# Optimization experiments

Hardware: AMD Instinct MI355X
Metric: run time of the kernel (lower is better)

## Reference

```python
import jax, jax.numpy as jnp
import numpy as np

B, N, K = 4, 2048, 30
NUM_PE, NUM_RBF, DIM_E = 16, 16, 128
EPS = 1e-6


def _normalize(x, axis=-1):
    # matches torch F.normalize (norm clamped to 1e-12)
    n = jnp.sqrt(jnp.sum(x * x, axis=axis, keepdims=True))
    return x / jnp.maximum(n, 1e-12)


def setup_inputs() -> dict:
    key = jax.random.key(0)
    k1, k2 = jax.random.split(key, 2)
    X = jax.random.normal(k1, (B, N, 3), dtype=jnp.float32)
    mask = jnp.ones((B, N), dtype=jnp.float32)
    W_e = jax.random.normal(k2, (NUM_PE + NUM_RBF + 7, DIM_E), dtype=jnp.float32) * 0.05
    b_e = jnp.zeros((DIM_E,), jnp.float32)
    gain = jnp.ones((DIM_E,), jnp.float32)
    bias = jnp.zeros((DIM_E,), jnp.float32)
    return {"X": X, "mask": mask, "W_e": W_e, "b_e": b_e, "gain": gain, "bias": bias}


def reference(X, mask, W_e, b_e, gain, bias):
    # ---- pairwise distances + topk neighbors ----
    mask2 = mask[:, :, None] * mask[:, None, :]                  # [B,N,N]
    dXp = X[:, :, None, :] - X[:, None, :, :]                    # [B,N,N,3]
    D = mask2 * jnp.sqrt(jnp.sum(dXp * dXp, -1) + EPS)
    D_max = jnp.max(D, -1, keepdims=True)
    D_adjust = D + (1.0 - mask2) * D_max
    negD, E_idx = jax.lax.top_k(-D_adjust, K)                    # K smallest
    D_neighbors = -negD                                          # [B,N,K]

    # ---- RBF ----
    D_mu = jnp.linspace(0.0, 20.0, NUM_RBF)
    D_sigma = 20.0 / NUM_RBF
    RBF = jnp.exp(-(((D_neighbors[..., None] - D_mu) / D_sigma) ** 2))  # [B,N,K,RBF]

    # ---- orientations (replicates source tensor_split indexing exactly) ----
    dX = X[:, 1:, :] - X[:, -1:, :]                              # [B,N-1,3] (broadcast vs last row)
    U = _normalize(dX)
    u_2 = U[:, :-2, :]
    u_1 = U[:, 1:-1, :]
    n_2 = _normalize(jnp.cross(u_2, u_1))
    o_1 = _normalize(u_2 - u_1)
    O = jnp.stack((o_1, n_2, jnp.cross(o_1, n_2)), -1)           # [B,N-3,3,3]
    O = O.reshape(O.shape[:-2] + (9,))
    O = jnp.pad(O, ((0, 0), (1, 2), (0, 0)))                     # [B,N,9]

    bidx = jnp.arange(B)[:, None, None]
    O_nb = O[bidx, E_idx].reshape(B, N, K, 3, 3)                 # gather_nodes(O)
    X_nb = X[bidx, E_idx]                                        # [B,N,K,3]
    O = O.reshape(B, N, 3, 3)

    dXn = X_nb - X[:, :, None, :]                                # [B,N,K,3]
    dU = _normalize(jnp.einsum('bnij,bnkj->bnki', O, dXn))       # O_i @ (x_k - x_i)
    R = jnp.einsum('bnji,bnkjl->bnkil', O, O_nb)                 # O_i^T @ O_k

    # ---- quaternions ----
    Rxx, Ryy, Rzz = R[..., 0, 0], R[..., 1, 1], R[..., 2, 2]
    mags = 0.5 * jnp.sqrt(jnp.abs(1.0 + jnp.stack(
        [Rxx - Ryy - Rzz, -Rxx + Ryy - Rzz, -Rxx - Ryy + Rzz], -1)))
    signs = jnp.sign(jnp.stack(
        [R[..., 2, 1] - R[..., 1, 2],
         R[..., 0, 2] - R[..., 2, 0],
         R[..., 1, 0] - R[..., 0, 1]], -1))
    w = jnp.sqrt(jax.nn.relu(1.0 + Rxx + Ryy + Rzz))[..., None] / 2.0
    Q = _normalize(jnp.concatenate((signs * mags, w), -1))       # [B,N,K,4]

    O_features = jnp.concatenate((dU, Q), -1)                    # [B,N,K,7]

    # ---- positional encodings ----
    ii = jnp.arange(N, dtype=jnp.float32)[None, :, None]
    d = (E_idx.astype(jnp.float32) - ii)[..., None]
    freq = jnp.exp(jnp.arange(0, NUM_PE, 2, dtype=jnp.float32) * (-np.log(10000.0) / NUM_PE))
    angles = d * freq
    E_pos = jnp.concatenate((jnp.cos(angles), jnp.sin(angles)), -1)  # [B,N,K,NUM_PE]

    # ---- linear + Normalize (LayerNorm with unbiased std) ----
    E = jnp.concatenate((E_pos, RBF, O_features), -1)            # [B,N,K,39]
    E = E @ W_e + b_e                                            # [B,N,K,DIM_E]
    mu = jnp.mean(E, -1, keepdims=True)
    sigma = jnp.std(E, axis=-1, keepdims=True, ddof=1)
    E = gain * (E - mu) / (sigma + EPS) + bias
    return E, E_idx
```

## Files before the change

### kernel.cpp

```cpp
#include <hip/hip_runtime.h>
#include <stdint.h>

#define Bv 4
#define Nv 2048
#define Kv 30
#define DIMv 128
#define NROW (Bv * Nv)
#define NEDGE (Bv * Nv * Kv)

__global__ __launch_bounds__(256) void o_kernel(const float* __restrict__ X,
                                                float* __restrict__ O9) {
    int id = blockIdx.x * 256 + threadIdx.x;
    if (id >= NROW) return;
    int b = id >> 11;
    int n = id & (Nv - 1);
    float o[9] = {0.f, 0.f, 0.f, 0.f, 0.f, 0.f, 0.f, 0.f, 0.f};
    if (n >= 1 && n <= Nv - 3) {
        const float* Xb = X + (size_t)b * Nv * 3;
        float lx = Xb[(Nv - 1) * 3 + 0], ly = Xb[(Nv - 1) * 3 + 1], lz = Xb[(Nv - 1) * 3 + 2];
        float ax = Xb[n * 3 + 0] - lx, ay = Xb[n * 3 + 1] - ly, az = Xb[n * 3 + 2] - lz;
        float bx = Xb[(n + 1) * 3 + 0] - lx, by = Xb[(n + 1) * 3 + 1] - ly, bz = Xb[(n + 1) * 3 + 2] - lz;
        float an = fmaxf(sqrtf(ax * ax + ay * ay + az * az), 1e-12f);
        ax /= an; ay /= an; az /= an;
        float bn = fmaxf(sqrtf(bx * bx + by * by + bz * bz), 1e-12f);
        bx /= bn; by /= bn; bz /= bn;
        float cx = ay * bz - az * by, cy = az * bx - ax * bz, cz = ax * by - ay * bx;
        float cn = fmaxf(sqrtf(cx * cx + cy * cy + cz * cz), 1e-12f);
        cx /= cn; cy /= cn; cz /= cn;
        float ox = ax - bx, oy = ay - by, oz = az - bz;
        float on = fmaxf(sqrtf(ox * ox + oy * oy + oz * oz), 1e-12f);
        ox /= on; oy /= on; oz /= on;
        float tx = oy * cz - oz * cy, ty = oz * cx - ox * cz, tz = ox * cy - oy * cx;
        o[0] = ox; o[1] = cx; o[2] = tx;
        o[3] = oy; o[4] = cy; o[5] = ty;
        o[6] = oz; o[7] = cz; o[8] = tz;
    }
#pragma unroll
    for (int i = 0; i < 9; ++i) O9[(size_t)id * 9 + i] = o[i];
}

__global__ __launch_bounds__(256) void topk_kernel(const float* __restrict__ X,
                                                   const float* __restrict__ mask,
                                                   int* __restrict__ idx_ws,
                                                   float* __restrict__ dn_ws,
                                                   float* __restrict__ idxf_out) {
    const int lane = threadIdx.x & 63;
    const int wv = threadIdx.x >> 6;
    const int row = blockIdx.x * 4 + wv;
    const int b = row >> 11;
    const int n = row & (Nv - 1);
    const float* Xb = X + (size_t)b * Nv * 3;
    const float* Mb = mask + (size_t)b * Nv;
    const float xn = Xb[n * 3 + 0], yn = Xb[n * 3 + 1], zn = Xb[n * 3 + 2];
    const float mi = Mb[n];

    float Dv[4][8];
    float dmax = 0.f;
#pragma unroll
    for (int gg = 0; gg < 4; ++gg)
#pragma unroll
        for (int s = 0; s < 8; ++s) {
            int j = (gg * 8 + s) * 64 + lane;
            float dx = __fsub_rn(xn, Xb[j * 3 + 0]);
            float dy = __fsub_rn(yn, Xb[j * 3 + 1]);
            float dz = __fsub_rn(zn, Xb[j * 3 + 2]);
            float ss = __fadd_rn(__fadd_rn(__fmul_rn(dx, dx), __fmul_rn(dy, dy)),
                                 __fmul_rn(dz, dz));
            float D = __fmul_rn(__fmul_rn(mi, Mb[j]), __fsqrt_rn(__fadd_rn(ss, 1e-6f)));
            Dv[gg][s] = D;
            dmax = fmaxf(dmax, D);
        }
#pragma unroll
    for (int m = 1; m < 64; m <<= 1) dmax = fmaxf(dmax, __shfl_xor(dmax, m, 64));

    uint32_t g[4][8];
    uint32_t gmv[4], gmw[4];
#pragma unroll
    for (int gg = 0; gg < 4; ++gg) {
#pragma unroll
        for (int s = 0; s < 8; ++s) {
            int j = (gg * 8 + s) * 64 + lane;
            float m2 = __fmul_rn(mi, Mb[j]);
            float adj = __fadd_rn(Dv[gg][s], __fmul_rn(__fsub_rn(1.f, m2), dmax));
            g[gg][s] = __float_as_uint(adj);
        }
        uint32_t nv = g[gg][0], nw = 0;
#pragma unroll
        for (int s = 1; s < 8; ++s)
            if (g[gg][s] < nv) { nv = g[gg][s]; nw = (uint32_t)s; }
        gmv[gg] = nv; gmw[gg] = nw;
    }

    const int rk = row * Kv;
    for (int p = 0; p < Kv; ++p) {
        uint32_t bv = gmv[0], bg = 0, bs = gmw[0];
        if (gmv[1] < bv) { bv = gmv[1]; bg = 1; bs = gmw[1]; }
        if (gmv[2] < bv) { bv = gmv[2]; bg = 2; bs = gmw[2]; }
        if (gmv[3] < bv) { bv = gmv[3]; bg = 3; bs = gmw[3]; }
        uint32_t myj = (((bg << 3) + bs) << 6) | (uint32_t)lane;

        uint32_t mv = bv;
#pragma unroll
        for (int m = 1; m < 64; m <<= 1) {
            uint32_t o = __shfl_xor(mv, m, 64);
            mv = (o < mv) ? o : mv;
        }
        uint32_t cand = (bv == mv) ? myj : 0xFFFFFFFFu;
#pragma unroll
        for (int m = 1; m < 64; m <<= 1) {
            uint32_t o = __shfl_xor(cand, m, 64);
            cand = (o < cand) ? o : cand;
        }
        const uint32_t mj = cand;

        if (lane == 0) {
            idx_ws[rk + p] = (int)mj;
            dn_ws[rk + p] = __uint_as_float(mv);
            idxf_out[rk + p] = (float)mj;
        }

        if ((mj & 63u) == (uint32_t)lane) {
            const uint32_t ww = mj >> 6;
            const uint32_t og = ww >> 3;
            const uint32_t os = ww & 7u;
#define RESCAN(G)                                                         \
            {                                                             \
                uint32_t nv = 0xFFFFFFFFu, nw = 0;                        \
                _Pragma("unroll")                                         \
                for (int s = 0; s < 8; ++s) {                             \
                    uint32_t val = ((uint32_t)s == os) ? 0xFFFFFFFFu      \
                                                       : g[G][s];         \
                    g[G][s] = val;                                        \
                    if (val < nv) { nv = val; nw = (uint32_t)s; }         \
                }                                                         \
                gmv[G] = nv; gmw[G] = nw;                                 \
            }
            if (og == 0) RESCAN(0)
            else if (og == 1) RESCAN(1)
            else if (og == 2) RESCAN(2)
            else RESCAN(3)
#undef RESCAN
        }
    }
}

__device__ __forceinline__ float sgnf(float x) {
    return (x > 0.f) ? 1.f : ((x < 0.f) ? -1.f : 0.f);
}

__global__ __launch_bounds__(256) void edge_kernel(const float* __restrict__ X,
                                                   const float* __restrict__ W,
                                                   const float* __restrict__ be,
                                                   const float* __restrict__ gain,
                                                   const float* __restrict__ bias,
                                                   const float* __restrict__ O9,
                                                   const int* __restrict__ idx_ws,
                                                   const float* __restrict__ dn_ws,
                                                   float* __restrict__ E) {
    __shared__ float fls[Kv][40];
    __shared__ float els[Kv][DIMv];
    __shared__ float sO[9];
    __shared__ float sX[3];
    __shared__ int   sidx[Kv];
    __shared__ float sdn[Kv];

    const int t = threadIdx.x;
    const int row = blockIdx.x;
    const int b = row >> 11;
    const int n = row & (Nv - 1);
    const int bN = b * Nv;
    const size_t ebase = (size_t)row * Kv;

    if (t < Kv) {
        sidx[t] = idx_ws[ebase + t];
        sdn[t] = dn_ws[ebase + t];
    } else if (t >= 32 && t < 41) {
        sO[t - 32] = O9[(size_t)row * 9 + (t - 32)];
    } else if (t >= 48 && t < 51) {
        sX[t - 48] = X[(size_t)row * 3 + (t - 48)];
    }
    __syncthreads();

    if (t < 240) {
        const int e = t >> 3;
        const int p = t & 7;
        const float c = -0.5756462732485115f;
        float freq = expf((float)(2 * p) * c);
        float ang = ((float)sidx[e] - (float)n) * freq;
        fls[e][p] = cosf(ang);
        fls[e][p + 8] = sinf(ang);
        float dn = sdn[e];
        float mu0 = (float)p * (20.0f / 15.0f);
        float z0 = (dn - mu0) * 0.8f;
        fls[e][16 + p] = expf(-z0 * z0);
        float mu1 = (float)(p + 8) * (20.0f / 15.0f);
        float z1 = (dn - mu1) * 0.8f;
        fls[e][24 + p] = expf(-z1 * z1);
    }
    if (t < Kv) {
        const int e = t;
        const int j = sidx[e];
        float oi[9], oj[9];
#pragma unroll
        for (int i = 0; i < 9; ++i) {
            oi[i] = sO[i];
            oj[i] = O9[((size_t)bN + j) * 9 + i];
        }
        float dx = X[((size_t)bN + j) * 3 + 0] - sX[0];
        float dy = X[((size_t)bN + j) * 3 + 1] - sX[1];
        float dz = X[((size_t)bN + j) * 3 + 2] - sX[2];
        float u0 = oi[0] * dx + oi[1] * dy + oi[2] * dz;
        float u1 = oi[3] * dx + oi[4] * dy + oi[5] * dz;
        float u2 = oi[6] * dx + oi[7] * dy + oi[8] * dz;
        float un = fmaxf(sqrtf(u0 * u0 + u1 * u1 + u2 * u2), 1e-12f);
        fls[e][32] = u0 / un;
        fls[e][33] = u1 / un;
        fls[e][34] = u2 / un;
        float R00 = oi[0] * oj[0] + oi[3] * oj[3] + oi[6] * oj[6];
        float R11 = oi[1] * oj[1] + oi[4] * oj[4] + oi[7] * oj[7];
        float R22 = oi[2] * oj[2] + oi[5] * oj[5] + oi[8] * oj[8];
        float R21 = oi[2] * oj[1] + oi[5] * oj[4] + oi[8] * oj[7];
        float R12 = oi[1] * oj[2] + oi[4] * oj[5] + oi[7] * oj[8];
        float R02 = oi[0] * oj[2] + oi[3] * oj[5] + oi[6] * oj[8];
        float R20 = oi[2] * oj[0] + oi[5] * oj[3] + oi[8] * oj[6];
        float R10 = oi[1] * oj[0] + oi[4] * oj[3] + oi[7] * oj[6];
        float R01 = oi[0] * oj[1] + oi[3] * oj[4] + oi[6] * oj[7];
        float m0 = 0.5f * sqrtf(fabsf(1.0f + (R00 - R11 - R22)));
        float m1 = 0.5f * sqrtf(fabsf(1.0f + (-R00 + R11 - R22)));
        float m2 = 0.5f * sqrtf(fabsf(1.0f + (-R00 - R11 + R22)));
        float s0 = sgnf(R21 - R12);
        float s1 = sgnf(R02 - R20);
        float s2 = sgnf(R10 - R01);
        float tr = 1.0f + R00 + R11 + R22;
        float w4 = sqrtf(fmaxf(tr, 0.f)) * 0.5f;
        float q0 = s0 * m0, q1 = s1 * m1, q2 = s2 * m2;
        float qn = fmaxf(sqrtf(q0 * q0 + q1 * q1 + q2 * q2 + w4 * w4), 1e-12f);
        fls[e][35] = q0 / qn;
        fls[e][36] = q1 / qn;
        fls[e][37] = q2 / qn;
        fls[e][38] = w4 / qn;
    }
    __syncthreads();

    {
        const int c = t & 127;
        const int h = t >> 7;
        float w[39];
#pragma unroll
        for (int i = 0; i < 39; ++i) w[i] = W[i * DIMv + c];
        const float bec = be[c];
        const int e0 = h * 15;
#pragma unroll 3
        for (int e = e0; e < e0 + 15; ++e) {
            const float* fr = &fls[e][0];
            float acc = bec;
#pragma unroll
            for (int q = 0; q < 9; ++q) {
                float4 v = *(const float4*)(fr + 4 * q);
                acc = fmaf(v.x, w[4 * q + 0], acc);
                acc = fmaf(v.y, w[4 * q + 1], acc);
                acc = fmaf(v.z, w[4 * q + 2], acc);
                acc = fmaf(v.w, w[4 * q + 3], acc);
            }
            acc = fmaf(fr[36], w[36], acc);
            acc = fmaf(fr[37], w[37], acc);
            acc = fmaf(fr[38], w[38], acc);
            els[e][c] = acc;
        }
    }
    __syncthreads();

    if (t < 240) {
        const int e = t >> 3;
        const int l = t & 7;
        const float* er = &els[e][l * 16];
        float vals[16];
        float s = 0.f;
#pragma unroll
        for (int q = 0; q < 4; ++q) {
            float4 v = *(const float4*)(er + 4 * q);
            vals[4 * q + 0] = v.x; vals[4 * q + 1] = v.y;
            vals[4 * q + 2] = v.z; vals[4 * q + 3] = v.w;
            s += v.x + v.y + v.z + v.w;
        }
        s += __shfl_xor(s, 1, 64);
        s += __shfl_xor(s, 2, 64);
        s += __shfl_xor(s, 4, 64);
        float mu = s * (1.0f / 128.0f);
        float vv = 0.f;
#pragma unroll
        for (int j = 0; j < 16; ++j) {
            float d = vals[j] - mu;
            vals[j] = d;
            vv += d * d;
        }
        vv += __shfl_xor(vv, 1, 64);
        vv += __shfl_xor(vv, 2, 64);
        vv += __shfl_xor(vv, 4, 64);
        float sigma = sqrtf(vv * (1.0f / 127.0f));
        float inv = 1.0f / (sigma + 1e-6f);
        float* out = E + (ebase + e) * DIMv + l * 16;
        const float* gp = gain + l * 16;
        const float* bp = bias + l * 16;
#pragma unroll
        for (int q = 0; q < 4; ++q) {
            float4 g = *(const float4*)(gp + 4 * q);
            float4 bb = *(const float4*)(bp + 4 * q);
            float4 r;
            r.x = g.x * vals[4 * q + 0] * inv + bb.x;
            r.y = g.y * vals[4 * q + 1] * inv + bb.y;
            r.z = g.z * vals[4 * q + 2] * inv + bb.z;
            r.w = g.w * vals[4 * q + 3] * inv + bb.w;
            *(float4*)(out + 4 * q) = r;
        }
    }
}

extern "C" void kernel_launch(void* const* d_in, const int* in_sizes, int n_in,
                              void* d_out, int out_size, void* d_ws, size_t ws_size,
                              hipStream_t stream) {
    const float* X = (const float*)d_in[0];
    const float* mask = (const float*)d_in[1];
    const float* W_e = (const float*)d_in[2];
    const float* b_e = (const float*)d_in[3];
    const float* gain = (const float*)d_in[4];
    const float* bias = (const float*)d_in[5];

    float* E = (float*)d_out;
    float* idxf = (float*)d_out + (size_t)NEDGE * DIMv;

    char* ws = (char*)d_ws;
    float* O9 = (float*)ws;
    int* idx_ws = (int*)(ws + (size_t)NROW * 9 * sizeof(float));
    float* dn_ws = (float*)(ws + (size_t)NROW * 9 * sizeof(float) +
                            (size_t)NEDGE * sizeof(int));

    hipLaunchKernelGGL(o_kernel, dim3((NROW + 255) / 256), dim3(256), 0, stream, X, O9);
    hipLaunchKernelGGL(topk_kernel, dim3(NROW / 4), dim3(256), 0, stream,
                       X, mask, idx_ws, dn_ws, idxf);
    hipLaunchKernelGGL(edge_kernel, dim3(NROW), dim3(256), 0, stream,
                       X, W_e, b_e, gain, bias, O9, idx_ws, dn_ws, E);
}
```

Before: 125.1 us.

## Pack top-k keys into 64-bit values and fuse linear with LayerNorm in registers

The top-k selection now packs each adjusted distance bits and column index into one 64-bit key. A single wave-wide min reduction then replaces the two separate reductions over value and index. In the edge kernel, each wave owns a set of edges and each lane computes two output channels, which removes the shared-memory staging buffer for the 128-wide linear output and one block barrier. LayerNorm statistics are reduced with full-wave shuffles and the output is written directly, at the cost of more weight registers per thread and scalar rather than float4 stores.

```diff
diff --git a/kernel.cpp b/kernel.cpp
--- a/kernel.cpp
+++ b/kernel.cpp
@@ -54,8 +54,8 @@
     const float xn = Xb[n * 3 + 0], yn = Xb[n * 3 + 1], zn = Xb[n * 3 + 2];
     const float mi = Mb[n];
 
-    float Dv[4][8];
-    float dmax = 0.f;
+    uint32_t a[4][8];
+    uint32_t bmax = 0;
 #pragma unroll
     for (int gg = 0; gg < 4; ++gg)
 #pragma unroll
@@ -67,55 +67,50 @@
             float ss = __fadd_rn(__fadd_rn(__fmul_rn(dx, dx), __fmul_rn(dy, dy)),
                                  __fmul_rn(dz, dz));
             float D = __fmul_rn(__fmul_rn(mi, Mb[j]), __fsqrt_rn(__fadd_rn(ss, 1e-6f)));
-            Dv[gg][s] = D;
-            dmax = fmaxf(dmax, D);
-        }
-#pragma unroll
-    for (int m = 1; m < 64; m <<= 1) dmax = fmaxf(dmax, __shfl_xor(dmax, m, 64));
-
-    uint32_t g[4][8];
-    uint32_t gmv[4], gmw[4];
+            uint32_t bits = __float_as_uint(D);
+            a[gg][s] = bits;
+            bmax = (bits > bmax) ? bits : bmax;
+        }
+#pragma unroll
+    for (int m = 1; m < 64; m <<= 1) {
+        uint32_t o = __shfl_xor(bmax, m, 64);
+        bmax = (o > bmax) ? o : bmax;
+    }
+    const float dmax = __uint_as_float(bmax);
+
+    unsigned long long gkey[4];
 #pragma unroll
     for (int gg = 0; gg < 4; ++gg) {
+        unsigned long long kmin = ~0ull;
 #pragma unroll
         for (int s = 0; s < 8; ++s) {
             int j = (gg * 8 + s) * 64 + lane;
             float m2 = __fmul_rn(mi, Mb[j]);
-            float adj = __fadd_rn(Dv[gg][s], __fmul_rn(__fsub_rn(1.f, m2), dmax));
-            g[gg][s] = __float_as_uint(adj);
-        }
-        uint32_t nv = g[gg][0], nw = 0;
-#pragma unroll
-        for (int s = 1; s < 8; ++s)
-            if (g[gg][s] < nv) { nv = g[gg][s]; nw = (uint32_t)s; }
-        gmv[gg] = nv; gmw[gg] = nw;
+            float adj = __fadd_rn(__uint_as_float(a[gg][s]),
+                                  __fmul_rn(__fsub_rn(1.f, m2), dmax));
+            uint32_t bits = __float_as_uint(adj);
+            a[gg][s] = bits;
+            unsigned long long kk = ((unsigned long long)bits << 32) | (unsigned)j;
+            kmin = (kk < kmin) ? kk : kmin;
+        }
+        gkey[gg] = kmin;
     }
 
     const int rk = row * Kv;
     for (int p = 0; p < Kv; ++p) {
-        uint32_t bv = gmv[0], bg = 0, bs = gmw[0];
-        if (gmv[1] < bv) { bv = gmv[1]; bg = 1; bs = gmw[1]; }
-        if (gmv[2] < bv) { bv = gmv[2]; bg = 2; bs = gmw[2]; }
-        if (gmv[3] < bv) { bv = gmv[3]; bg = 3; bs = gmw[3]; }
-        uint32_t myj = (((bg << 3) + bs) << 6) | (uint32_t)lane;
-
-        uint32_t mv = bv;
+        unsigned long long k0 = (gkey[0] < gkey[1]) ? gkey[0] : gkey[1];
+        unsigned long long k1 = (gkey[2] < gkey[3]) ? gkey[2] : gkey[3];
+        unsigned long long key = (k0 < k1) ? k0 : k1;
 #pragma unroll
         for (int m = 1; m < 64; m <<= 1) {
-            uint32_t o = __shfl_xor(mv, m, 64);
-            mv = (o < mv) ? o : mv;
-        }
-        uint32_t cand = (bv == mv) ? myj : 0xFFFFFFFFu;
-#pragma unroll
-        for (int m = 1; m < 64; m <<= 1) {
-            uint32_t o = __shfl_xor(cand, m, 64);
-            cand = (o < cand) ? o : cand;
-        }
-        const uint32_t mj = cand;
+            unsigned long long o = __shfl_xor(key, m, 64);
+            key = (o < key) ? o : key;
+        }
+        const uint32_t mj = (uint32_t)(key & 0xFFFFFFFFull);
 
         if (lane == 0) {
             idx_ws[rk + p] = (int)mj;
-            dn_ws[rk + p] = __uint_as_float(mv);
+            dn_ws[rk + p] = __uint_as_float((uint32_t)(key >> 32));
             idxf_out[rk + p] = (float)mj;
         }
 
@@ -123,17 +118,19 @@
             const uint32_t ww = mj >> 6;
             const uint32_t og = ww >> 3;
             const uint32_t os = ww & 7u;
-#define RESCAN(G)                                                         \
-            {                                                             \
-                uint32_t nv = 0xFFFFFFFFu, nw = 0;                        \
-                _Pragma("unroll")                                         \
-                for (int s = 0; s < 8; ++s) {                             \
-                    uint32_t val = ((uint32_t)s == os) ? 0xFFFFFFFFu      \
-                                                       : g[G][s];         \
-                    g[G][s] = val;                                        \
-                    if (val < nv) { nv = val; nw = (uint32_t)s; }         \
-                }                                                         \
-                gmv[G] = nv; gmw[G] = nw;                                 \
+#define RESCAN(G)                                                              \
+            {                                                                  \
+                unsigned long long kmin = ~0ull;                               \
+                _Pragma("unroll")                                              \
+                for (int s = 0; s < 8; ++s) {                                  \
+                    uint32_t val = ((uint32_t)s == os) ? 0xFFFFFFFFu           \
+                                                       : a[G][s];              \
+                    a[G][s] = val;                                             \
+                    unsigned long long kk = ((unsigned long long)val << 32) |  \
+                        (unsigned)((((G) * 8 + s) << 6) | lane);               \
+                    kmin = (kk < kmin) ? kk : kmin;                            \
+                }                                                              \
+                gkey[G] = kmin;                                                \
             }
             if (og == 0) RESCAN(0)
             else if (og == 1) RESCAN(1)
@@ -158,13 +155,14 @@
                                                    const float* __restrict__ dn_ws,
                                                    float* __restrict__ E) {
     __shared__ float fls[Kv][40];
-    __shared__ float els[Kv][DIMv];
     __shared__ float sO[9];
     __shared__ float sX[3];
     __shared__ int   sidx[Kv];
     __shared__ float sdn[Kv];
 
     const int t = threadIdx.x;
+    const int lane = t & 63;
+    const int w = t >> 6;
     const int row = blockIdx.x;
     const int b = row >> 11;
     const int n = row & (Nv - 1);
@@ -239,79 +237,57 @@
         fls[e][36] = q1 / qn;
         fls[e][37] = q2 / qn;
         fls[e][38] = w4 / qn;
+        fls[e][39] = 0.f;
     }
     __syncthreads();
 
-    {
-        const int c = t & 127;
-        const int h = t >> 7;
-        float w[39];
-#pragma unroll
-        for (int i = 0; i < 39; ++i) w[i] = W[i * DIMv + c];
-        const float bec = be[c];
-        const int e0 = h * 15;
-#pragma unroll 3
-        for (int e = e0; e < e0 + 15; ++e) {
-            const float* fr = &fls[e][0];
-            float acc = bec;
-#pragma unroll
-            for (int q = 0; q < 9; ++q) {
+    const int c0 = lane, c1 = lane + 64;
+    float w0[40], w1[40];
+#pragma unroll
+    for (int i = 0; i < 39; ++i) {
+        w0[i] = W[i * DIMv + c0];
+        w1[i] = W[i * DIMv + c1];
+    }
+    w0[39] = 0.f; w1[39] = 0.f;
+    const float be0 = be[c0], be1 = be[c1];
+    const float g0 = gain[c0], g1 = gain[c1];
+    const float bb0 = bias[c0], bb1 = bias[c1];
+    const int off = (w < 2) ? w * 8 : 16 + (w - 2) * 7;
+    const int cnt = (w < 2) ? 8 : 7;
+
+    float a0[8], a1[8];
+#pragma unroll
+    for (int k = 0; k < 8; ++k) {
+        if (k < cnt) {
+            const float* fr = &fls[off + k][0];
+            float s0 = be0, s1 = be1;
+#pragma unroll
+            for (int q = 0; q < 10; ++q) {
                 float4 v = *(const float4*)(fr + 4 * q);
-                acc = fmaf(v.x, w[4 * q + 0], acc);
-                acc = fmaf(v.y, w[4 * q + 1], acc);
-                acc = fmaf(v.z, w[4 * q + 2], acc);
-                acc = fmaf(v.w, w[4 * q + 3], acc);
+                s0 = fmaf(v.x, w0[4 * q + 0], s0); s1 = fmaf(v.x, w1[4 * q + 0], s1);
+                s0 = fmaf(v.y, w0[4 * q + 1], s0); s1 = fmaf(v.y, w1[4 * q + 1], s1);
+                s0 = fmaf(v.z, w0[4 * q + 2], s0); s1 = fmaf(v.z, w1[4 * q + 2], s1);
+                s0 = fmaf(v.w, w0[4 * q + 3], s0); s1 = fmaf(v.w, w1[4 * q + 3], s1);
             }
-            acc = fmaf(fr[36], w[36], acc);
-            acc = fmaf(fr[37], w[37], acc);
-            acc = fmaf(fr[38], w[38], acc);
-            els[e][c] = acc;
-        }
-    }
-    __syncthreads();
-
-    if (t < 240) {
-        const int e = t >> 3;
-        const int l = t & 7;
-        const float* er = &els[e][l * 16];
-        float vals[16];
-        float s = 0.f;
-#pragma unroll
-        for (int q = 0; q < 4; ++q) {
-            float4 v = *(const float4*)(er + 4 * q);
-            vals[4 * q + 0] = v.x; vals[4 * q + 1] = v.y;
-            vals[4 * q + 2] = v.z; vals[4 * q + 3] = v.w;
-            s += v.x + v.y + v.z + v.w;
-        }
-        s += __shfl_xor(s, 1, 64);
-        s += __shfl_xor(s, 2, 64);
-        s += __shfl_xor(s, 4, 64);
-        float mu = s * (1.0f / 128.0f);
-        float vv = 0.f;
-#pragma unroll
-        for (int j = 0; j < 16; ++j) {
-            float d = vals[j] - mu;
-            vals[j] = d;
-            vv += d * d;
-        }
-        vv += __shfl_xor(vv, 1, 64);
-        vv += __shfl_xor(vv, 2, 64);
-        vv += __shfl_xor(vv, 4, 64);
-        float sigma = sqrtf(vv * (1.0f / 127.0f));
-        float inv = 1.0f / (sigma + 1e-6f);
-        float* out = E + (ebase + e) * DIMv + l * 16;
-        const float* gp = gain + l * 16;
-        const float* bp = bias + l * 16;
-#pragma unroll
-        for (int q = 0; q < 4; ++q) {
-            float4 g = *(const float4*)(gp + 4 * q);
-            float4 bb = *(const float4*)(bp + 4 * q);
-            float4 r;
-            r.x = g.x * vals[4 * q + 0] * inv + bb.x;
-            r.y = g.y * vals[4 * q + 1] * inv + bb.y;
-            r.z = g.z * vals[4 * q + 2] * inv + bb.z;
-            r.w = g.w * vals[4 * q + 3] * inv + bb.w;
-            *(float4*)(out + 4 * q) = r;
+            a0[k] = s0; a1[k] = s1;
+        }
+    }
+
+#pragma unroll
+    for (int k = 0; k < 8; ++k) {
+        if (k < cnt) {
+            float s = a0[k] + a1[k];
+#pragma unroll
+            for (int m = 1; m < 64; m <<= 1) s += __shfl_xor(s, m, 64);
+            float mu = s * (1.0f / 128.0f);
+            float d0 = a0[k] - mu, d1 = a1[k] - mu;
+            float vv = d0 * d0 + d1 * d1;
+#pragma unroll
+            for (int m = 1; m < 64; m <<= 1) vv += __shfl_xor(vv, m, 64);
+            float inv = 1.0f / (sqrtf(vv * (1.0f / 127.0f)) + 1e-6f);
+            float* out = E + (ebase + off + k) * DIMv;
+            out[c0] = g0 * d0 * inv + bb0;
+            out[c1] = g1 * d1 * inv + bb1;
         }
     }
 }
```

Result: slower. 212.4 us (+69.8%).
